# Performance work log

Hardware: AMD Instinct MI355X
Metric: run time of the kernel (lower is better)

The kernel has to match this reference:

```python
import jax, jax.numpy as jnp
import numpy as np

BSZ, E, D, R = 8, 40000, 128, 512
NUM_STEPS, K, DEG = 2, 3, 64
T = E * DEG  # uniform out-degree KB
M = K * DEG  # max gathered triples per example per step


def setup_inputs() -> dict:
    key = jax.random.key(0)
    ks = jax.random.split(key, 10)
    s = 1.0 / np.sqrt(D)
    start_idx = jax.random.randint(ks[0], (BSZ,), 0, E)
    start = jnp.zeros((BSZ, E), jnp.float32).at[jnp.arange(BSZ), start_idx].set(1.0)
    query = jax.random.randint(ks[1], (BSZ,), 0, R)
    sub = jnp.repeat(jnp.arange(E), DEG)
    obj = jax.random.randint(ks[2], (T,), 0, E)
    rel = jax.random.randint(ks[3], (T,), 0, R)
    kb_triple = jnp.stack([sub, obj, rel], axis=1)  # [T,3] = (sub, obj, rel)
    kb_range = jnp.stack([jnp.arange(E) * DEG, (jnp.arange(E) + 1) * DEG], axis=1)
    rel_emb = jax.random.normal(ks[4], (R, D), jnp.float32) * s
    step_W = jax.random.normal(ks[5], (NUM_STEPS, D, D), jnp.float32) * np.sqrt(2.0 / D)
    step_b = jnp.zeros((NUM_STEPS, D), jnp.float32)
    gru_W_ih = jax.random.normal(ks[6], (3 * D, D), jnp.float32) * s
    gru_W_hh = jax.random.normal(ks[7], (3 * D, D), jnp.float32) * s
    gru_b_ih = jnp.zeros((3 * D,), jnp.float32)
    gru_b_hh = jnp.zeros((3 * D,), jnp.float32)
    cls_w = jax.random.normal(ks[8], (D,), jnp.float32) * np.sqrt(2.0 / D)
    cls_b = jnp.zeros((1,), jnp.float32)
    return dict(start=start, rel_emb=rel_emb, step_W=step_W, step_b=step_b,
                gru_W_ih=gru_W_ih, gru_W_hh=gru_W_hh, gru_b_ih=gru_b_ih, gru_b_hh=gru_b_hh,
                cls_w=cls_w, cls_b=cls_b, query=query, kb_triple=kb_triple, kb_range=kb_range)


def _gru_cell(x, h, W_ih, W_hh, b_ih, b_hh):
    # torch GRU cell, gate order (r, z, n). x, h: [..., D]
    gi = x @ W_ih.T + b_ih
    gh = h @ W_hh.T + b_hh
    i_r, i_z, i_n = jnp.split(gi, 3, axis=-1)
    h_r, h_z, h_n = jnp.split(gh, 3, axis=-1)
    r = jax.nn.sigmoid(i_r + h_r)
    z = jax.nn.sigmoid(i_z + h_z)
    n = jnp.tanh(i_n + r * h_n)
    return (1.0 - z) * n + z * h


def _forward(start, rel_emb, step_W, step_b, gru_W_ih, gru_W_hh, gru_b_ih, gru_b_hh,
             cls_w, cls_b, query, kb_triple, kb_range):
    bsz, nE = start.shape
    d = rel_emb.shape[1]
    q_emb = rel_emb[query]                       # [bsz, D]
    last_e = start
    hist = jnp.zeros((bsz, nE, d), start.dtype)  # [bsz, E, D]
    for t in range(NUM_STEPS):
        cq = jnp.tanh(q_emb @ step_W[t] + step_b[t])           # [bsz, D]
        _, top_idx = jax.lax.top_k(last_e, K)                  # [bsz, K]
        n_valid = 1 if t == 0 else K                           # topk=1 at step 0
        ent_mask = jnp.arange(K) < n_valid                     # [K]
        lo = kb_range[top_idx, 0]                              # [bsz, K]
        hi = kb_range[top_idx, 1]
        tri_idx = lo[..., None] + jnp.arange(DEG)              # [bsz, K, DEG]
        valid = (tri_idx < hi[..., None]) & ent_mask[None, :, None]
        tri_idx = jnp.where(valid, tri_idx, 0).reshape(bsz, M)
        valid = valid.reshape(bsz, M).astype(start.dtype)
        trip = kb_triple[tri_idx]                              # [bsz, M, 3]
        sub, obj, rel = trip[..., 0], trip[..., 1], trip[..., 2]
        sub_feat = jnp.take_along_axis(hist, sub[..., None], axis=1)   # [bsz, M, D]
        rel_feat = rel_emb[rel]                                        # [bsz, M, D]
        trans = _gru_cell(rel_feat, sub_feat, gru_W_ih, gru_W_hh, gru_b_ih, gru_b_hh)
        trans_prob = jax.nn.sigmoid(jnp.einsum('bmd,d->bm', trans * cq[:, None, :], cls_w) + cls_b[0])
        sub_p = jnp.take_along_axis(last_e, sub, axis=1)       # [bsz, M]
        obj_p = sub_p * trans_prob * valid                     # masked transition prob
        last_e = jax.vmap(lambda o, p: jnp.zeros((nE,), p.dtype).at[o].add(p))(obj, obj_p)
        obj_feat = trans * obj_p[..., None]
        hist = jax.vmap(lambda o, f: jnp.zeros((nE, d), f.dtype).at[o].add(f))(obj, obj_feat)
        zdiv = jax.lax.stop_gradient(jnp.where(last_e > 1.0, last_e, 1.0))
        last_e = last_e / zdiv
    return last_e


def reference(start, rel_emb, step_W, step_b, gru_W_ih, gru_W_hh, gru_b_ih, gru_b_hh,
              cls_w, cls_b, query, kb_triple, kb_range):
    return _forward(start, rel_emb, step_W, step_b, gru_W_ih, gru_W_hh, gru_b_ih, gru_b_hh,
                    cls_w, cls_b, query, kb_triple, kb_range)
```

## Files before the change

kernel.cpp:

```cpp
#include <hip/hip_runtime.h>
#include <math.h>

#define BSZ 8
#define E_ENT 40000
#define D_DIM 128
#define K_TOP 3
#define DEG 64
#define D3 (3 * D_DIM)
#define NCH 40
#define CHUNK 1000

typedef unsigned long long ull;

__device__ __forceinline__ float sigmoidf_(float x) { return 1.0f / (1.0f + expf(-x)); }

__device__ __forceinline__ ull make_key(float v, int idx) {
    return ((ull)__float_as_uint(v) << 32) |
           (ull)(0xFFFFFFFFu - (unsigned int)idx);
}

__global__ void transpose_kernel(const float* __restrict__ W_ih,
                                 const float* __restrict__ W_hh,
                                 float* __restrict__ WT_ih,
                                 float* __restrict__ WT_hh) {
    int i = blockIdx.x * blockDim.x + threadIdx.x;
    if (i >= D3 * D_DIM) return;
    int row = i / D_DIM, col = i % D_DIM;
    WT_ih[col * D3 + row] = W_ih[row * D_DIM + col];
    WT_hh[col * D3 + row] = W_hh[row * D_DIM + col];
}

__global__ void cq_kernel(const float* __restrict__ rel_emb,
                          const float* __restrict__ step_W,
                          const float* __restrict__ step_b,
                          const int* __restrict__ query,
                          float* __restrict__ cq) {
    int t = blockIdx.x / BSZ, b = blockIdx.x % BSZ;
    int d = threadIdx.x;
    __shared__ float xs[D_DIM];
    xs[d] = rel_emb[query[b] * D_DIM + d];
    __syncthreads();
    float acc = step_b[t * D_DIM + d];
    const float* W = step_W + t * D_DIM * D_DIM;
    for (int k = 0; k < D_DIM; k++) acc += xs[k] * W[k * D_DIM + d];
    cq[(t * BSZ + b) * D_DIM + d] = tanhf(acc);
}

__global__ void topk_stageA(const float* __restrict__ e, ull* __restrict__ keys) {
    int blk = blockIdx.x;
    int b = blk / NCH, c = blk % NCH;
    int tid = threadIdx.x;
    const float* row = e + (size_t)b * E_ENT;
    int base = c * CHUNK;
    __shared__ ull red[256];
    __shared__ ull pick[K_TOP];
    for (int p = 0; p < K_TOP; p++) {
        ull best = 0ull;
        for (int i = tid; i < CHUNK; i += 256) {
            int idx = base + i;
            ull k = make_key(row[idx], idx);
            bool skip = false;
            for (int q = 0; q < p; q++) if (pick[q] == k) skip = true;
            if (!skip && k > best) best = k;
        }
        red[tid] = best;
        __syncthreads();
        for (int s = 128; s > 0; s >>= 1) {
            if (tid < s && red[tid + s] > red[tid]) red[tid] = red[tid + s];
            __syncthreads();
        }
        if (tid == 0) { pick[p] = red[0]; keys[(b * NCH + c) * K_TOP + p] = red[0]; }
        __syncthreads();
    }
}

__global__ void topk_stageB(const ull* __restrict__ keys,
                            int* __restrict__ out_idx, float* __restrict__ out_val) {
    int b = blockIdx.x, tid = threadIdx.x;
    __shared__ ull sk[NCH * K_TOP];
    __shared__ ull red[128];
    __shared__ ull pick[K_TOP];
    if (tid < NCH * K_TOP) sk[tid] = keys[b * NCH * K_TOP + tid];
    __syncthreads();
    for (int p = 0; p < K_TOP; p++) {
        ull best = 0ull;
        if (tid < NCH * K_TOP) {
            ull k = sk[tid];
            bool skip = false;
            for (int q = 0; q < p; q++) if (pick[q] == k) skip = true;
            if (!skip) best = k;
        }
        red[tid] = best;
        __syncthreads();
        for (int s = 64; s > 0; s >>= 1) {
            if (tid < s && red[tid + s] > red[tid]) red[tid] = red[tid + s];
            __syncthreads();
        }
        if (tid == 0) {
            pick[p] = red[0];
            out_idx[b * K_TOP + p] = (int)(0xFFFFFFFFu - (unsigned int)(red[0] & 0xFFFFFFFFull));
            out_val[b * K_TOP + p] = __uint_as_float((unsigned int)(red[0] >> 32));
        }
        __syncthreads();
    }
}

__global__ void cand_topk(const int* __restrict__ objs, const float* __restrict__ p0,
                          int* __restrict__ out_idx, float* __restrict__ out_val) {
    int b = blockIdx.x, m = threadIdx.x;
    __shared__ int so[DEG];
    __shared__ float sp[DEG];
    __shared__ ull red[DEG];
    __shared__ int picked[K_TOP];
    so[m] = objs[b * DEG + m];
    sp[m] = p0[b * DEG + m];
    __syncthreads();
    int o = so[m];
    float v = 0.f;
    for (int i = 0; i < DEG; i++) if (so[i] == o) v += sp[i];
    v = v / fmaxf(v, 1.0f);
    ull key = make_key(v, o);
    for (int p = 0; p < K_TOP; p++) {
        ull k2 = key;
        for (int q = 0; q < p; q++) if (picked[q] == o) k2 = 0ull;
        red[m] = k2;
        __syncthreads();
        for (int s = 32; s > 0; s >>= 1) {
            if (m < s && red[m + s] > red[m]) red[m] = red[m + s];
            __syncthreads();
        }
        if (m == 0) {
            ull best = red[0];
            int idx = (int)(0xFFFFFFFFu - (unsigned int)(best & 0xFFFFFFFFull));
            float val = __uint_as_float((unsigned int)(best >> 32));
            if (idx < 0 || idx >= E_ENT) { idx = p; val = 0.f; }
            picked[p] = idx;
            out_idx[b * K_TOP + p] = idx;
            out_val[b * K_TOP + p] = val;
        }
        __syncthreads();
    }
}

__global__ void step_kernel(int t, int nk,
                            const int* __restrict__ top_idx,
                            const float* __restrict__ top_val,
                            const float* __restrict__ cq,
                            const float* __restrict__ rel_emb,
                            const int* __restrict__ kb_triple,
                            const int* __restrict__ kb_range,
                            const float* __restrict__ WT_ih,
                            const float* __restrict__ WT_hh,
                            const float* __restrict__ b_ih,
                            const float* __restrict__ b_hh,
                            const float* __restrict__ cls_w,
                            const float* __restrict__ cls_b,
                            const float* __restrict__ feat_in,
                            const int* __restrict__ obj_in,
                            float* __restrict__ feat_out,
                            int* __restrict__ obj_out,
                            float* __restrict__ p_out,
                            float* __restrict__ e_out) {
    int blk = blockIdx.x;
    int b = blk / (nk * DEG);
    int rem = blk % (nk * DEG);
    int k = rem / DEG;
    int j = rem % DEG;
    int d = threadIdx.x;

    int ent = top_idx[b * K_TOP + k];
    float sub_p = top_val[b * K_TOP + k];
    int lo = kb_range[2 * ent], hi = kb_range[2 * ent + 1];
    int tri = lo + j;
    bool vj = (tri < hi);
    int tuse = vj ? tri : 0;
    int sub = kb_triple[3 * tuse + 0];
    int obj = kb_triple[3 * tuse + 1];
    int rel = kb_triple[3 * tuse + 2];

    __shared__ float xs[D_DIM];
    __shared__ float hs[D_DIM];
    __shared__ float red[D_DIM];

    xs[d] = rel_emb[rel * D_DIM + d];
    float hd = 0.f;
    if (t > 0) {
        const int* ob = obj_in + b * DEG;
        const float* fb = feat_in + (size_t)b * DEG * D_DIM;
        for (int m = 0; m < DEG; m++) {
            if (ob[m] == sub) hd += fb[m * D_DIM + d];
        }
    }
    hs[d] = hd;
    __syncthreads();

    float ir = b_ih[d], iz = b_ih[D_DIM + d], inn = b_ih[2 * D_DIM + d];
    float hr = b_hh[d], hz = b_hh[D_DIM + d], hn = b_hh[2 * D_DIM + d];
    if (t > 0) {
        for (int kk = 0; kk < D_DIM; kk++) {
            float xk = xs[kk], hk = hs[kk];
            const float* wi = WT_ih + kk * D3;
            const float* wh = WT_hh + kk * D3;
            ir += xk * wi[d]; iz += xk * wi[D_DIM + d]; inn += xk * wi[2 * D_DIM + d];
            hr += hk * wh[d]; hz += hk * wh[D_DIM + d]; hn += hk * wh[2 * D_DIM + d];
        }
    } else {
        for (int kk = 0; kk < D_DIM; kk++) {
            float xk = xs[kk];
            const float* wi = WT_ih + kk * D3;
            ir += xk * wi[d]; iz += xk * wi[D_DIM + d]; inn += xk * wi[2 * D_DIM + d];
        }
    }
    float r = sigmoidf_(ir + hr);
    float z = sigmoidf_(iz + hz);
    float n = tanhf(inn + r * hn);
    float trans = (1.f - z) * n + z * hd;

    red[d] = trans * cq[b * D_DIM + d] * cls_w[d];
    __syncthreads();
    for (int s = 64; s > 0; s >>= 1) {
        if (d < s) red[d] += red[d + s];
        __syncthreads();
    }
    float prob = sigmoidf_(red[0] + cls_b[0]);
    float obj_p = vj ? sub_p * prob : 0.f;

    if (t == 0) {
        feat_out[((size_t)b * DEG + rem) * D_DIM + d] = trans * obj_p;
        if (d == 0) {
            obj_out[b * DEG + rem] = obj;
            p_out[b * DEG + rem] = obj_p;
        }
    } else if (d == 0 && obj_p != 0.f) {
        atomicAdd(&e_out[(size_t)b * E_ENT + obj], obj_p);
    }
}

__global__ void norm_kernel(float* __restrict__ e) {
    int i = blockIdx.x * blockDim.x + threadIdx.x;
    if (i < BSZ * E_ENT) {
        float v = e[i];
        e[i] = v / (v > 1.0f ? v : 1.0f);
    }
}

extern "C" void kernel_launch(void* const* d_in, const int* in_sizes, int n_in,
                              void* d_out, int out_size, void* d_ws, size_t ws_size,
                              hipStream_t stream) {
    const float* start    = (const float*)d_in[0];
    const float* rel_emb  = (const float*)d_in[1];
    const float* step_W   = (const float*)d_in[2];
    const float* step_b   = (const float*)d_in[3];
    const float* W_ih     = (const float*)d_in[4];
    const float* W_hh     = (const float*)d_in[5];
    const float* b_ih     = (const float*)d_in[6];
    const float* b_hh     = (const float*)d_in[7];
    const float* cls_w    = (const float*)d_in[8];
    const float* cls_b    = (const float*)d_in[9];
    const int*   query    = (const int*)d_in[10];
    const int*   kb_triple = (const int*)d_in[11];
    const int*   kb_range  = (const int*)d_in[12];
    float* out = (float*)d_out;

    char* ws = (char*)d_ws;
    float* WT_ih = (float*)ws;  ws += (size_t)D3 * D_DIM * sizeof(float);
    float* WT_hh = (float*)ws;  ws += (size_t)D3 * D_DIM * sizeof(float);
    float* cq    = (float*)ws;  ws += (size_t)2 * BSZ * D_DIM * sizeof(float);
    float* feat  = (float*)ws;  ws += (size_t)BSZ * DEG * D_DIM * sizeof(float);
    int*   objs  = (int*)ws;    ws += (size_t)BSZ * DEG * sizeof(int);
    float* p0    = (float*)ws;  ws += (size_t)BSZ * DEG * sizeof(float);
    ull*   keysA = (ull*)ws;    ws += (size_t)BSZ * NCH * K_TOP * sizeof(ull);
    int*   idx0  = (int*)ws;    ws += (size_t)BSZ * K_TOP * sizeof(int);
    float* val0  = (float*)ws;  ws += (size_t)BSZ * K_TOP * sizeof(float);
    int*   idx1  = (int*)ws;    ws += (size_t)BSZ * K_TOP * sizeof(int);
    float* val1  = (float*)ws;  ws += (size_t)BSZ * K_TOP * sizeof(float);

    transpose_kernel<<<(D3 * D_DIM + 255) / 256, 256, 0, stream>>>(W_ih, W_hh, WT_ih, WT_hh);
    cq_kernel<<<2 * BSZ, D_DIM, 0, stream>>>(rel_emb, step_W, step_b, query, cq);

    topk_stageA<<<BSZ * NCH, 256, 0, stream>>>(start, keysA);
    topk_stageB<<<BSZ, 128, 0, stream>>>(keysA, idx0, val0);
    step_kernel<<<BSZ * DEG, D_DIM, 0, stream>>>(
        0, 1, idx0, val0, cq, rel_emb, kb_triple, kb_range,
        WT_ih, WT_hh, b_ih, b_hh, cls_w, cls_b,
        nullptr, nullptr, feat, objs, p0, nullptr);

    cand_topk<<<BSZ, DEG, 0, stream>>>(objs, p0, idx1, val1);
    hipMemsetAsync(d_out, 0, (size_t)BSZ * E_ENT * sizeof(float), stream);
    step_kernel<<<BSZ * K_TOP * DEG, D_DIM, 0, stream>>>(
        1, K_TOP, idx1, val1, cq + BSZ * D_DIM, rel_emb, kb_triple, kb_range,
        WT_ih, WT_hh, b_ih, b_hh, cls_w, cls_b,
        feat, objs, nullptr, nullptr, nullptr, out);
    norm_kernel<<<(BSZ * E_ENT + 255) / 256, 256, 0, stream>>>(out);
}
```

Measured before the change: 63.99 us.

## Fuse prep kernels, batch triples per block, replace atomics+norm with finalize

Merges the weight transpose, cq projection, output zeroing and top-k stage A into a single prep launch. Because the start vector is one-hot, top-1 per chunk is enough, so stage B is folded into step0. The candidate top-k is recomputed inside each step1 block. Each block now handles 8 triples, so every weight load is reused across 8 GRU inputs. The global atomic scatter plus full-array normalisation pass is replaced by a per-example finalize kernel that sums duplicate objects and writes only touched entries. Fewer launches and less redundant weight traffic are expected, in exchange for redundant top-k work per block and reliance on the one-hot start.

```diff
diff --git a/kernel.cpp b/kernel.cpp
--- a/kernel.cpp
+++ b/kernel.cpp
@@ -6,9 +6,18 @@
 #define D_DIM 128
 #define K_TOP 3
 #define DEG 64
+#define M_TRI (K_TOP * DEG)
 #define D3 (3 * D_DIM)
 #define NCH 40
 #define CHUNK 1000
+#define EPB 8
+#define G_PER (DEG / EPB)
+
+#define ZERO_BLOCKS 313
+#define TR_BLOCKS 192
+#define CQ_BLOCKS (2 * BSZ)
+#define SA_BLOCKS (BSZ * NCH)
+#define PREP_BLOCKS (ZERO_BLOCKS + TR_BLOCKS + CQ_BLOCKS + SA_BLOCKS)
 
 typedef unsigned long long ull;
 
@@ -18,50 +27,57 @@
     return ((ull)__float_as_uint(v) << 32) |
            (ull)(0xFFFFFFFFu - (unsigned int)idx);
 }
-
-__global__ void transpose_kernel(const float* __restrict__ W_ih,
-                                 const float* __restrict__ W_hh,
-                                 float* __restrict__ WT_ih,
-                                 float* __restrict__ WT_hh) {
-    int i = blockIdx.x * blockDim.x + threadIdx.x;
-    if (i >= D3 * D_DIM) return;
-    int row = i / D_DIM, col = i % D_DIM;
-    WT_ih[col * D3 + row] = W_ih[row * D_DIM + col];
-    WT_hh[col * D3 + row] = W_hh[row * D_DIM + col];
-}
-
-__global__ void cq_kernel(const float* __restrict__ rel_emb,
-                          const float* __restrict__ step_W,
-                          const float* __restrict__ step_b,
-                          const int* __restrict__ query,
-                          float* __restrict__ cq) {
-    int t = blockIdx.x / BSZ, b = blockIdx.x % BSZ;
-    int d = threadIdx.x;
+__device__ __forceinline__ int key_idx(ull k) {
+    return (int)(0xFFFFFFFFu - (unsigned int)(k & 0xFFFFFFFFull));
+}
+__device__ __forceinline__ float key_val(ull k) {
+    return __uint_as_float((unsigned int)(k >> 32));
+}
+
+__global__ void prep_kernel(const float* __restrict__ start,
+                            const float* __restrict__ rel_emb,
+                            const float* __restrict__ step_W,
+                            const float* __restrict__ step_b,
+                            const int* __restrict__ query,
+                            const float* __restrict__ W_ih,
+                            const float* __restrict__ W_hh,
+                            float* __restrict__ WT_ih,
+                            float* __restrict__ WT_hh,
+                            float* __restrict__ cq,
+                            ull* __restrict__ keysA,
+                            float* __restrict__ out) {
+    int blk = blockIdx.x, tid = threadIdx.x;
     __shared__ float xs[D_DIM];
-    xs[d] = rel_emb[query[b] * D_DIM + d];
-    __syncthreads();
-    float acc = step_b[t * D_DIM + d];
-    const float* W = step_W + t * D_DIM * D_DIM;
-    for (int k = 0; k < D_DIM; k++) acc += xs[k] * W[k * D_DIM + d];
-    cq[(t * BSZ + b) * D_DIM + d] = tanhf(acc);
-}
-
-__global__ void topk_stageA(const float* __restrict__ e, ull* __restrict__ keys) {
-    int blk = blockIdx.x;
-    int b = blk / NCH, c = blk % NCH;
-    int tid = threadIdx.x;
-    const float* row = e + (size_t)b * E_ENT;
-    int base = c * CHUNK;
     __shared__ ull red[256];
-    __shared__ ull pick[K_TOP];
-    for (int p = 0; p < K_TOP; p++) {
+    if (blk < ZERO_BLOCKS) {
+        int i = blk * 256 + tid;
+        if (i < (BSZ * E_ENT) / 4) ((float4*)out)[i] = float4{0.f, 0.f, 0.f, 0.f};
+    } else if (blk < ZERO_BLOCKS + TR_BLOCKS) {
+        int i = (blk - ZERO_BLOCKS) * 256 + tid;
+        int row = i / D_DIM, col = i % D_DIM;
+        WT_ih[col * D3 + row] = W_ih[row * D_DIM + col];
+        WT_hh[col * D3 + row] = W_hh[row * D_DIM + col];
+    } else if (blk < ZERO_BLOCKS + TR_BLOCKS + CQ_BLOCKS) {
+        int g = blk - (ZERO_BLOCKS + TR_BLOCKS);
+        int t = g / BSZ, b = g % BSZ;
+        if (tid < D_DIM) xs[tid] = rel_emb[query[b] * D_DIM + tid];
+        __syncthreads();
+        if (tid < D_DIM) {
+            float acc = step_b[t * D_DIM + tid];
+            const float* W = step_W + t * D_DIM * D_DIM;
+            for (int k = 0; k < D_DIM; k++) acc += xs[k] * W[k * D_DIM + tid];
+            cq[(t * BSZ + b) * D_DIM + tid] = tanhf(acc);
+        }
+    } else {
+        int g = blk - (ZERO_BLOCKS + TR_BLOCKS + CQ_BLOCKS);
+        int b = g / NCH, c = g % NCH;
+        const float* row = start + (size_t)b * E_ENT;
+        int base = c * CHUNK;
         ull best = 0ull;
         for (int i = tid; i < CHUNK; i += 256) {
             int idx = base + i;
             ull k = make_key(row[idx], idx);
-            bool skip = false;
-            for (int q = 0; q < p; q++) if (pick[q] == k) skip = true;
-            if (!skip && k > best) best = k;
+            if (k > best) best = k;
         }
         red[tid] = best;
         __syncthreads();
@@ -69,179 +85,224 @@
             if (tid < s && red[tid + s] > red[tid]) red[tid] = red[tid + s];
             __syncthreads();
         }
-        if (tid == 0) { pick[p] = red[0]; keys[(b * NCH + c) * K_TOP + p] = red[0]; }
-        __syncthreads();
-    }
-}
-
-__global__ void topk_stageB(const ull* __restrict__ keys,
-                            int* __restrict__ out_idx, float* __restrict__ out_val) {
-    int b = blockIdx.x, tid = threadIdx.x;
-    __shared__ ull sk[NCH * K_TOP];
-    __shared__ ull red[128];
-    __shared__ ull pick[K_TOP];
-    if (tid < NCH * K_TOP) sk[tid] = keys[b * NCH * K_TOP + tid];
-    __syncthreads();
-    for (int p = 0; p < K_TOP; p++) {
-        ull best = 0ull;
-        if (tid < NCH * K_TOP) {
-            ull k = sk[tid];
-            bool skip = false;
-            for (int q = 0; q < p; q++) if (pick[q] == k) skip = true;
-            if (!skip) best = k;
-        }
-        red[tid] = best;
-        __syncthreads();
-        for (int s = 64; s > 0; s >>= 1) {
-            if (tid < s && red[tid + s] > red[tid]) red[tid] = red[tid + s];
-            __syncthreads();
-        }
-        if (tid == 0) {
-            pick[p] = red[0];
-            out_idx[b * K_TOP + p] = (int)(0xFFFFFFFFu - (unsigned int)(red[0] & 0xFFFFFFFFull));
-            out_val[b * K_TOP + p] = __uint_as_float((unsigned int)(red[0] >> 32));
-        }
-        __syncthreads();
-    }
-}
-
-__global__ void cand_topk(const int* __restrict__ objs, const float* __restrict__ p0,
-                          int* __restrict__ out_idx, float* __restrict__ out_val) {
-    int b = blockIdx.x, m = threadIdx.x;
+        if (tid == 0) keysA[b * NCH + c] = red[0];
+    }
+}
+
+__global__ __launch_bounds__(128) void step0_kernel(
+        const ull* __restrict__ keysA,
+        const float* __restrict__ cq,
+        const float* __restrict__ rel_emb,
+        const int* __restrict__ kb_triple,
+        const int* __restrict__ kb_range,
+        const float* __restrict__ WT_ih,
+        const float* __restrict__ b_ih,
+        const float* __restrict__ b_hh,
+        const float* __restrict__ cls_w,
+        const float* __restrict__ cls_b,
+        float* __restrict__ feat_out,
+        int* __restrict__ obj_out,
+        float* __restrict__ p_out) {
+    int blk = blockIdx.x;
+    int b = blk / G_PER, g = blk % G_PER;
+    int d = threadIdx.x;
+
+    __shared__ ull red[64];
+    __shared__ float xs[EPB][D_DIM];
+    __shared__ float part[EPB][2];
+    __shared__ float probs[EPB];
+
+    if (d < 64) red[d] = (d < NCH) ? keysA[b * NCH + d] : 0ull;
+    __syncthreads();
+    for (int s = 32; s > 0; s >>= 1) {
+        if (d < s && red[d + s] > red[d]) red[d] = red[d + s];
+        __syncthreads();
+    }
+    int ent = key_idx(red[0]);
+    float sub_p = key_val(red[0]);
+    int lo = kb_range[2 * ent], hi = kb_range[2 * ent + 1];
+
+    int objl[EPB]; bool vj[EPB];
+    for (int e = 0; e < EPB; e++) {
+        int j = g * EPB + e, tri = lo + j;
+        vj[e] = tri < hi;
+        int tuse = vj[e] ? tri : 0;
+        objl[e] = kb_triple[3 * tuse + 1];
+        int rel = kb_triple[3 * tuse + 2];
+        xs[e][d] = rel_emb[rel * D_DIM + d];
+    }
+    __syncthreads();
+
+    float bhr = b_hh[d], bhz = b_hh[D_DIM + d], bhn = b_hh[2 * D_DIM + d];
+    float ir[EPB], iz[EPB], inn[EPB];
+    {
+        float bir = b_ih[d], biz = b_ih[D_DIM + d], bin = b_ih[2 * D_DIM + d];
+        for (int e = 0; e < EPB; e++) { ir[e] = bir; iz[e] = biz; inn[e] = bin; }
+    }
+    for (int kk = 0; kk < D_DIM; kk++) {
+        const float* wi = WT_ih + kk * D3;
+        float wr = wi[d], wz = wi[D_DIM + d], wn = wi[2 * D_DIM + d];
+        #pragma unroll
+        for (int e = 0; e < EPB; e++) {
+            float xk = xs[e][kk];
+            ir[e] += xk * wr; iz[e] += xk * wz; inn[e] += xk * wn;
+        }
+    }
+    float cqd = cq[b * D_DIM + d] * cls_w[d];
+    float trans[EPB];
+    for (int e = 0; e < EPB; e++) {
+        float r = sigmoidf_(ir[e] + bhr);
+        float z = sigmoidf_(iz[e] + bhz);
+        float n = tanhf(inn[e] + r * bhn);
+        trans[e] = (1.f - z) * n;
+        float v = trans[e] * cqd;
+        for (int off = 32; off > 0; off >>= 1) v += __shfl_xor(v, off, 64);
+        if ((d & 63) == 0) part[e][d >> 6] = v;
+    }
+    __syncthreads();
+    if (d < EPB) probs[d] = sigmoidf_(part[d][0] + part[d][1] + cls_b[0]);
+    __syncthreads();
+    for (int e = 0; e < EPB; e++) {
+        int j = g * EPB + e;
+        float obj_p = vj[e] ? sub_p * probs[e] : 0.f;
+        feat_out[((size_t)b * DEG + j) * D_DIM + d] = trans[e] * obj_p;
+        if (d == 0) { obj_out[b * DEG + j] = objl[e]; p_out[b * DEG + j] = obj_p; }
+    }
+}
+
+__global__ __launch_bounds__(128) void step1_kernel(
+        const int* __restrict__ objs,
+        const float* __restrict__ p0,
+        const float* __restrict__ feat_in,
+        const float* __restrict__ cq,
+        const float* __restrict__ rel_emb,
+        const int* __restrict__ kb_triple,
+        const int* __restrict__ kb_range,
+        const float* __restrict__ WT_ih,
+        const float* __restrict__ WT_hh,
+        const float* __restrict__ b_ih,
+        const float* __restrict__ b_hh,
+        const float* __restrict__ cls_w,
+        const float* __restrict__ cls_b,
+        int* __restrict__ obj_out,
+        float* __restrict__ p_out) {
+    int blk = blockIdx.x;
+    int b = blk / (K_TOP * G_PER);
+    int rem = blk % (K_TOP * G_PER);
+    int k = rem / G_PER, g = rem % G_PER;
+    int d = threadIdx.x;
+
     __shared__ int so[DEG];
     __shared__ float sp[DEG];
-    __shared__ ull red[DEG];
-    __shared__ int picked[K_TOP];
-    so[m] = objs[b * DEG + m];
-    sp[m] = p0[b * DEG + m];
+    __shared__ ull red[64];
+    __shared__ int pick_i[K_TOP];
+    __shared__ float pick_v[K_TOP];
+    __shared__ float hds[D_DIM];
+    __shared__ float xs[EPB][D_DIM];
+    __shared__ float part[EPB][2];
+    __shared__ float probs[EPB];
+
+    if (d < DEG) { so[d] = objs[b * DEG + d]; sp[d] = p0[b * DEG + d]; }
+    __syncthreads();
+
+    ull mykey = 0ull; int myobj = -1;
+    if (d < DEG) {
+        myobj = so[d];
+        float v = 0.f;
+        for (int i = 0; i < DEG; i++) if (so[i] == myobj) v += sp[i];
+        v = v / fmaxf(v, 1.f);
+        mykey = make_key(v, myobj);
+    }
+    for (int p = 0; p < K_TOP; p++) {
+        ull k2 = mykey;
+        for (int q = 0; q < p; q++) if (myobj == pick_i[q]) k2 = 0ull;
+        if (d < 64) red[d] = k2;
+        __syncthreads();
+        for (int s = 32; s > 0; s >>= 1) {
+            if (d < s && red[d + s] > red[d]) red[d] = red[d + s];
+            __syncthreads();
+        }
+        if (d == 0) {
+            int idx = key_idx(red[0]);
+            float val = key_val(red[0]);
+            if (idx < 0 || idx >= E_ENT) { idx = p; val = 0.f; }
+            pick_i[p] = idx; pick_v[p] = val;
+        }
+        __syncthreads();
+    }
+    int ent = pick_i[k];
+    float sub_p = pick_v[k];
+
+    float hd = 0.f;
+    for (int m = 0; m < DEG; m++)
+        if (so[m] == ent) hd += feat_in[((size_t)b * DEG + m) * D_DIM + d];
+    hds[d] = hd;
+
+    int lo = kb_range[2 * ent], hi = kb_range[2 * ent + 1];
+    int objl[EPB]; bool vj[EPB];
+    for (int e = 0; e < EPB; e++) {
+        int j = g * EPB + e, tri = lo + j;
+        vj[e] = tri < hi;
+        int tuse = vj[e] ? tri : 0;
+        objl[e] = kb_triple[3 * tuse + 1];
+        int rel = kb_triple[3 * tuse + 2];
+        xs[e][d] = rel_emb[rel * D_DIM + d];
+    }
+    __syncthreads();
+
+    float hr = b_hh[d], hz = b_hh[D_DIM + d], hn = b_hh[2 * D_DIM + d];
+    float ir[EPB], iz[EPB], inn[EPB];
+    {
+        float bir = b_ih[d], biz = b_ih[D_DIM + d], bin = b_ih[2 * D_DIM + d];
+        for (int e = 0; e < EPB; e++) { ir[e] = bir; iz[e] = biz; inn[e] = bin; }
+    }
+    for (int kk = 0; kk < D_DIM; kk++) {
+        const float* wi = WT_ih + kk * D3;
+        const float* wh = WT_hh + kk * D3;
+        float wr = wi[d], wz = wi[D_DIM + d], wn = wi[2 * D_DIM + d];
+        float hk = hds[kk];
+        hr += hk * wh[d]; hz += hk * wh[D_DIM + d]; hn += hk * wh[2 * D_DIM + d];
+        #pragma unroll
+        for (int e = 0; e < EPB; e++) {
+            float xk = xs[e][kk];
+            ir[e] += xk * wr; iz[e] += xk * wz; inn[e] += xk * wn;
+        }
+    }
+    float cqd = cq[b * D_DIM + d] * cls_w[d];
+    for (int e = 0; e < EPB; e++) {
+        float r = sigmoidf_(ir[e] + hr);
+        float z = sigmoidf_(iz[e] + hz);
+        float n = tanhf(inn[e] + r * hn);
+        float trans = (1.f - z) * n + z * hd;
+        float v = trans * cqd;
+        for (int off = 32; off > 0; off >>= 1) v += __shfl_xor(v, off, 64);
+        if ((d & 63) == 0) part[e][d >> 6] = v;
+    }
+    __syncthreads();
+    if (d < EPB) probs[d] = sigmoidf_(part[d][0] + part[d][1] + cls_b[0]);
+    __syncthreads();
+    if (d == 0) {
+        for (int e = 0; e < EPB; e++) {
+            int idx = b * M_TRI + k * DEG + g * EPB + e;
+            obj_out[idx] = objl[e];
+            p_out[idx] = vj[e] ? sub_p * probs[e] : 0.f;
+        }
+    }
+}
+
+__global__ void finalize_kernel(const int* __restrict__ obj1,
+                                const float* __restrict__ p1,
+                                float* __restrict__ out) {
+    int b = blockIdx.x, m = threadIdx.x;
+    __shared__ int so[M_TRI];
+    __shared__ float sp[M_TRI];
+    so[m] = obj1[b * M_TRI + m];
+    sp[m] = p1[b * M_TRI + m];
     __syncthreads();
     int o = so[m];
     float v = 0.f;
-    for (int i = 0; i < DEG; i++) if (so[i] == o) v += sp[i];
-    v = v / fmaxf(v, 1.0f);
-    ull key = make_key(v, o);
-    for (int p = 0; p < K_TOP; p++) {
-        ull k2 = key;
-        for (int q = 0; q < p; q++) if (picked[q] == o) k2 = 0ull;
-        red[m] = k2;
-        __syncthreads();
-        for (int s = 32; s > 0; s >>= 1) {
-            if (m < s && red[m + s] > red[m]) red[m] = red[m + s];
-            __syncthreads();
-        }
-        if (m == 0) {
-            ull best = red[0];
-            int idx = (int)(0xFFFFFFFFu - (unsigned int)(best & 0xFFFFFFFFull));
-            float val = __uint_as_float((unsigned int)(best >> 32));
-            if (idx < 0 || idx >= E_ENT) { idx = p; val = 0.f; }
-            picked[p] = idx;
-            out_idx[b * K_TOP + p] = idx;
-            out_val[b * K_TOP + p] = val;
-        }
-        __syncthreads();
-    }
-}
-
-__global__ void step_kernel(int t, int nk,
-                            const int* __restrict__ top_idx,
-                            const float* __restrict__ top_val,
-                            const float* __restrict__ cq,
-                            const float* __restrict__ rel_emb,
-                            const int* __restrict__ kb_triple,
-                            const int* __restrict__ kb_range,
-                            const float* __restrict__ WT_ih,
-                            const float* __restrict__ WT_hh,
-                            const float* __restrict__ b_ih,
-                            const float* __restrict__ b_hh,
-                            const float* __restrict__ cls_w,
-                            const float* __restrict__ cls_b,
-                            const float* __restrict__ feat_in,
-                            const int* __restrict__ obj_in,
-                            float* __restrict__ feat_out,
-                            int* __restrict__ obj_out,
-                            float* __restrict__ p_out,
-                            float* __restrict__ e_out) {
-    int blk = blockIdx.x;
-    int b = blk / (nk * DEG);
-    int rem = blk % (nk * DEG);
-    int k = rem / DEG;
-    int j = rem % DEG;
-    int d = threadIdx.x;
-
-    int ent = top_idx[b * K_TOP + k];
-    float sub_p = top_val[b * K_TOP + k];
-    int lo = kb_range[2 * ent], hi = kb_range[2 * ent + 1];
-    int tri = lo + j;
-    bool vj = (tri < hi);
-    int tuse = vj ? tri : 0;
-    int sub = kb_triple[3 * tuse + 0];
-    int obj = kb_triple[3 * tuse + 1];
-    int rel = kb_triple[3 * tuse + 2];
-
-    __shared__ float xs[D_DIM];
-    __shared__ float hs[D_DIM];
-    __shared__ float red[D_DIM];
-
-    xs[d] = rel_emb[rel * D_DIM + d];
-    float hd = 0.f;
-    if (t > 0) {
-        const int* ob = obj_in + b * DEG;
-        const float* fb = feat_in + (size_t)b * DEG * D_DIM;
-        for (int m = 0; m < DEG; m++) {
-            if (ob[m] == sub) hd += fb[m * D_DIM + d];
-        }
-    }
-    hs[d] = hd;
-    __syncthreads();
-
-    float ir = b_ih[d], iz = b_ih[D_DIM + d], inn = b_ih[2 * D_DIM + d];
-    float hr = b_hh[d], hz = b_hh[D_DIM + d], hn = b_hh[2 * D_DIM + d];
-    if (t > 0) {
-        for (int kk = 0; kk < D_DIM; kk++) {
-            float xk = xs[kk], hk = hs[kk];
-            const float* wi = WT_ih + kk * D3;
-            const float* wh = WT_hh + kk * D3;
-            ir += xk * wi[d]; iz += xk * wi[D_DIM + d]; inn += xk * wi[2 * D_DIM + d];
-            hr += hk * wh[d]; hz += hk * wh[D_DIM + d]; hn += hk * wh[2 * D_DIM + d];
-        }
-    } else {
-        for (int kk = 0; kk < D_DIM; kk++) {
-            float xk = xs[kk];
-            const float* wi = WT_ih + kk * D3;
-            ir += xk * wi[d]; iz += xk * wi[D_DIM + d]; inn += xk * wi[2 * D_DIM + d];
-        }
-    }
-    float r = sigmoidf_(ir + hr);
-    float z = sigmoidf_(iz + hz);
-    float n = tanhf(inn + r * hn);
-    float trans = (1.f - z) * n + z * hd;
-
-    red[d] = trans * cq[b * D_DIM + d] * cls_w[d];
-    __syncthreads();
-    for (int s = 64; s > 0; s >>= 1) {
-        if (d < s) red[d] += red[d + s];
-        __syncthreads();
-    }
-    float prob = sigmoidf_(red[0] + cls_b[0]);
-    float obj_p = vj ? sub_p * prob : 0.f;
-
-    if (t == 0) {
-        feat_out[((size_t)b * DEG + rem) * D_DIM + d] = trans * obj_p;
-        if (d == 0) {
-            obj_out[b * DEG + rem] = obj;
-            p_out[b * DEG + rem] = obj_p;
-        }
-    } else if (d == 0 && obj_p != 0.f) {
-        atomicAdd(&e_out[(size_t)b * E_ENT + obj], obj_p);
-    }
-}
-
-__global__ void norm_kernel(float* __restrict__ e) {
-    int i = blockIdx.x * blockDim.x + threadIdx.x;
-    if (i < BSZ * E_ENT) {
-        float v = e[i];
-        e[i] = v / (v > 1.0f ? v : 1.0f);
-    }
+    for (int i = 0; i < M_TRI; i++) if (so[i] == o) v += sp[i];
+    out[(size_t)b * E_ENT + o] = v / fmaxf(v, 1.f);
 }
 
 extern "C" void kernel_launch(void* const* d_in, const int* in_sizes, int n_in,
@@ -269,27 +330,23 @@
     float* feat  = (float*)ws;  ws += (size_t)BSZ * DEG * D_DIM * sizeof(float);
     int*   objs  = (int*)ws;    ws += (size_t)BSZ * DEG * sizeof(int);
     float* p0    = (float*)ws;  ws += (size_t)BSZ * DEG * sizeof(float);
-    ull*   keysA = (ull*)ws;    ws += (size_t)BSZ * NCH * K_TOP * sizeof(ull);
-    int*   idx0  = (int*)ws;    ws += (size_t)BSZ * K_TOP * sizeof(int);
-    float* val0  = (float*)ws;  ws += (size_t)BSZ * K_TOP * sizeof(float);
-    int*   idx1  = (int*)ws;    ws += (size_t)BSZ * K_TOP * sizeof(int);
-    float* val1  = (float*)ws;  ws += (size_t)BSZ * K_TOP * sizeof(float);
-
-    transpose_kernel<<<(D3 * D_DIM + 255) / 256, 256, 0, stream>>>(W_ih, W_hh, WT_ih, WT_hh);
-    cq_kernel<<<2 * BSZ, D_DIM, 0, stream>>>(rel_emb, step_W, step_b, query, cq);
-
-    topk_stageA<<<BSZ * NCH, 256, 0, stream>>>(start, keysA);
-    topk_stageB<<<BSZ, 128, 0, stream>>>(keysA, idx0, val0);
-    step_kernel<<<BSZ * DEG, D_DIM, 0, stream>>>(
-        0, 1, idx0, val0, cq, rel_emb, kb_triple, kb_range,
+    ull*   keysA = (ull*)ws;    ws += (size_t)BSZ * NCH * sizeof(ull);
+    int*   obj1  = (int*)ws;    ws += (size_t)BSZ * M_TRI * sizeof(int);
+    float* p1    = (float*)ws;  ws += (size_t)BSZ * M_TRI * sizeof(float);
+
+    prep_kernel<<<PREP_BLOCKS, 256, 0, stream>>>(
+        start, rel_emb, step_W, step_b, query, W_ih, W_hh,
+        WT_ih, WT_hh, cq, keysA, out);
+
+    step0_kernel<<<BSZ * G_PER, 128, 0, stream>>>(
+        keysA, cq, rel_emb, kb_triple, kb_range,
+        WT_ih, b_ih, b_hh, cls_w, cls_b,
+        feat, objs, p0);
+
+    step1_kernel<<<BSZ * K_TOP * G_PER, 128, 0, stream>>>(
+        objs, p0, feat, cq + BSZ * D_DIM, rel_emb, kb_triple, kb_range,
         WT_ih, WT_hh, b_ih, b_hh, cls_w, cls_b,
-        nullptr, nullptr, feat, objs, p0, nullptr);
-
-    cand_topk<<<BSZ, DEG, 0, stream>>>(objs, p0, idx1, val1);
-    hipMemsetAsync(d_out, 0, (size_t)BSZ * E_ENT * sizeof(float), stream);
-    step_kernel<<<BSZ * K_TOP * DEG, D_DIM, 0, stream>>>(
-        1, K_TOP, idx1, val1, cq + BSZ * D_DIM, rel_emb, kb_triple, kb_range,
-        WT_ih, WT_hh, b_ih, b_hh, cls_w, cls_b,
-        feat, objs, nullptr, nullptr, nullptr, out);
-    norm_kernel<<<(BSZ * E_ENT + 255) / 256, 256, 0, stream>>>(out);
-}
+        obj1, p1);
+
+    finalize_kernel<<<BSZ, M_TRI, 0, stream>>>(obj1, p1, out);
+}
```

Measured after the change: 79.41 us. 24.1% more time.
